# Kernel optimization log

Hardware: AMD Instinct MI355X
Metric: run time of the kernel (lower is better)

Reference implementation:

```python
import jax, jax.numpy as jnp
import numpy as np

N_WIRES = 8
DIM = 1 << N_WIRES  # 256
ENC_WIRES = [0, 1, 2, 2, 4, 5, 6, 7]  # faithful to source: wire 2 twice, wire 3 skipped

# Precompute composed CNOT-ring permutation: CNOT(0,1),(1,2),...,(6,7),(7,0)
_idx = np.arange(DIM)
_perm = _idx.copy()
for c, t in [(k, k + 1) for k in range(N_WIRES - 1)] + [(N_WIRES - 1, 0)]:
    cbit = (_idx >> (N_WIRES - 1 - c)) & 1
    P = np.where(cbit == 1, _idx ^ (1 << (N_WIRES - 1 - t)), _idx)
    _perm = _perm[P]
CNOT_PERM = jnp.asarray(_perm)
# Pauli-Z sign table per wire: (8, 256)
Z_SIGNS = jnp.asarray(1 - 2 * ((_idx[None, :] >> (N_WIRES - 1 - np.arange(N_WIRES)[:, None])) & 1)).astype(jnp.float32)


def _rx(state, wire, theta):
    """Apply RX(theta) on `wire`. state: (N, 256) complex64, theta: (N,) float."""
    N = state.shape[0]
    s = state.reshape(N, 1 << wire, 2, 1 << (N_WIRES - 1 - wire))
    half = theta * 0.5
    c = jnp.cos(half)[:, None, None]
    sn = jnp.sin(half)[:, None, None]
    a, b = s[:, :, 0, :], s[:, :, 1, :]
    top = c * a - 1j * sn * b
    bot = -1j * sn * a + c * b
    return jnp.stack([top, bot], axis=2).reshape(N, DIM)


def qlayer(tokens, theta):
    """Batched 8-qubit circuit: encoder RX(x_k), trainable RX(theta_w), CNOT ring, <Z_w>.
    tokens: (N, 8) float32 -> (N, 8) float32 expectation values."""
    N = tokens.shape[0]
    state = jnp.zeros((N, DIM), jnp.complex64).at[:, 0].set(1.0)
    for k, w in enumerate(ENC_WIRES):
        state = _rx(state, w, tokens[:, k])
    for w in range(N_WIRES):
        state = _rx(state, w, jnp.broadcast_to(theta[w], (N,)))
    state = state[:, CNOT_PERM]
    probs = state.real ** 2 + state.imag ** 2  # (N, 256)
    return probs @ Z_SIGNS.T  # (N, 8)


def setup_inputs() -> dict:
    key = jax.random.key(0)
    kx, kt = jax.random.split(key)
    x = jax.random.normal(kx, (16, 1024, 8), dtype=jnp.float32)
    theta = jax.random.uniform(kt, (8,), dtype=jnp.float32, minval=0.0, maxval=2.0 * np.pi)
    return {"x": x, "theta": theta}


def reference(x, theta):
    B, S, E = x.shape
    H, dk = 2, E // 2
    tok = x.reshape(B * S, E)
    # Original computes Q, K, V with the SAME shared q_layer on the SAME input,
    # so Q == K == V; compute once.
    qkv = qlayer(tok, theta).reshape(B, S, E)
    h = qkv.reshape(B, S, H, dk).transpose(0, 2, 1, 3)  # (B,H,S,dk)
    scores = jnp.einsum('bhqd,bhkd->bhqk', h, h) / np.sqrt(dk).astype(np.float32)
    w = jax.nn.softmax(scores, axis=-1)  # (eval mode: dropout inactive)
    attn = jnp.einsum('bhqk,bhkd->bhqd', w, h)
    concat = attn.transpose(0, 2, 1, 3).reshape(B, S, E)
    out = qlayer(concat.reshape(B * S, E), theta).reshape(B, S, E)
    return out
```

## Files before the change

kernel.cpp:

```cpp
#include <hip/hip_runtime.h>

#define SEQ 1024

typedef __attribute__((ext_vector_type(2))) float f2;

static __device__ __forceinline__ int lds_addr(int k) {
    return (k << 3) + ((k >> 4) << 2);
}

static __device__ __forceinline__ void qrow(const float th[8], const float y[8], float o[8]) {
    float a[8];
    a[0] = y[0] + th[0];
    a[1] = y[1] + th[1];
    a[2] = y[2] + y[3] + th[2];
    a[3] = th[3];
    a[4] = y[4] + th[4];
    a[5] = y[5] + th[5];
    a[6] = y[6] + th[6];
    a[7] = y[7] + th[7];
    float c[8];
#pragma unroll
    for (int w = 0; w < 8; ++w) c[w] = __cosf(a[w]);
    o[1] = c[0] * c[1];
#pragma unroll
    for (int w = 2; w < 8; ++w) o[w] = o[w - 1] * c[w];
    float s = c[7];
#pragma unroll
    for (int w = 6; w >= 1; --w) s *= c[w];
    o[0] = s;
}

__global__ __launch_bounds__(256, 4) void mhaq_fused(const float* __restrict__ x,
                                                     const float* __restrict__ theta,
                                                     float* __restrict__ out) {
    __shared__ __align__(16) float h_lds[8448];

    const int b   = blockIdx.x >> 6;
    const int qof = (blockIdx.x & 63) << 4;
    const int t   = threadIdx.x;

    float th[8];
#pragma unroll
    for (int w = 0; w < 8; ++w) th[w] = theta[w];

    const float4* xb = (const float4*)(x + (size_t)b * SEQ * 8);
    float4 v0[4], v1[4];
#pragma unroll
    for (int r = 0; r < 4; ++r) {
        const int k = t + (r << 8);
        v0[r] = xb[2 * k];
        v1[r] = xb[2 * k + 1];
    }
#pragma unroll
    for (int r = 0; r < 4; ++r) {
        const int k = t + (r << 8);
        const float y[8] = {v0[r].x, v0[r].y, v0[r].z, v0[r].w,
                            v1[r].x, v1[r].y, v1[r].z, v1[r].w};
        float o[8];
        qrow(th, y, o);
        float4* p = (float4*)&h_lds[lds_addr(k)];
        p[0] = make_float4(o[0], o[1], o[2], o[3]);
        p[1] = make_float4(o[4], o[5], o[6], o[7]);
    }
    __syncthreads();

    const int lane  = t & 63;
    const int wv    = t >> 6;
    const int qbase = qof + (wv << 2);

    const float qscale = 0.5f * 1.44269504f;
    f2 qv[4][4];
#pragma unroll
    for (int qq = 0; qq < 4; ++qq) {
        const float* qp = &h_lds[lds_addr(qbase + qq)];
        qv[qq][0] = f2{qp[0], qp[1]} * qscale;
        qv[qq][1] = f2{qp[2], qp[3]} * qscale;
        qv[qq][2] = f2{qp[4], qp[5]} * qscale;
        qv[qq][3] = f2{qp[6], qp[7]} * qscale;
    }

    float l0[4] = {0.f, 0.f, 0.f, 0.f};
    float l1[4] = {0.f, 0.f, 0.f, 0.f};
    f2 a01[4], a23[4], a45[4], a67[4];
#pragma unroll
    for (int qq = 0; qq < 4; ++qq) {
        a01[qq] = f2{0.f, 0.f};
        a23[qq] = f2{0.f, 0.f};
        a45[qq] = f2{0.f, 0.f};
        a67[qq] = f2{0.f, 0.f};
    }

    int base = lds_addr(lane << 4);
#pragma unroll 4
    for (int i = 0; i < 16; ++i) {
        const float4 k0 = *(const float4*)&h_lds[base];
        const float4 k1 = *(const float4*)&h_lds[base + 4];
        base += 8;
        const f2 k01 = {k0.x, k0.y}, k23 = {k0.z, k0.w};
        const f2 k45 = {k1.x, k1.y}, k67 = {k1.z, k1.w};
#pragma unroll
        for (int qq = 0; qq < 4; ++qq) {
            const f2 d0 = qv[qq][0] * k01 + qv[qq][1] * k23;
            const f2 d1 = qv[qq][2] * k45 + qv[qq][3] * k67;
            const float e0 = __builtin_amdgcn_exp2f(d0.x + d0.y);
            const float e1 = __builtin_amdgcn_exp2f(d1.x + d1.y);
            l0[qq] += e0;
            l1[qq] += e1;
            const f2 e0v = {e0, e0}, e1v = {e1, e1};
            a01[qq] += e0v * k01;
            a23[qq] += e0v * k23;
            a45[qq] += e1v * k45;
            a67[qq] += e1v * k67;
        }
    }

    float red[40];
#pragma unroll
    for (int qq = 0; qq < 4; ++qq) {
        red[qq * 10 + 0] = l0[qq];
        red[qq * 10 + 1] = l1[qq];
        red[qq * 10 + 2] = a01[qq].x;
        red[qq * 10 + 3] = a01[qq].y;
        red[qq * 10 + 4] = a23[qq].x;
        red[qq * 10 + 5] = a23[qq].y;
        red[qq * 10 + 6] = a45[qq].x;
        red[qq * 10 + 7] = a45[qq].y;
        red[qq * 10 + 8] = a67[qq].x;
        red[qq * 10 + 9] = a67[qq].y;
    }
#pragma unroll
    for (int m = 1; m < 64; m <<= 1) {
#pragma unroll
        for (int j = 0; j < 40; ++j) red[j] += __shfl_xor(red[j], m);
    }

    float sel[10];
#pragma unroll
    for (int j = 0; j < 10; ++j) {
        const float v01 = (lane & 1) ? red[10 + j] : red[j];
        const float v23 = (lane & 1) ? red[30 + j] : red[20 + j];
        sel[j] = (lane & 2) ? v23 : v01;
    }
    if (lane < 4) {
        const float inv0 = 1.0f / sel[0];
        const float inv1 = 1.0f / sel[1];
        float y[8];
#pragma unroll
        for (int d = 0; d < 4; ++d) {
            y[d]     = sel[2 + d] * inv0;
            y[4 + d] = sel[6 + d] * inv1;
        }
        float o[8];
        qrow(th, y, o);
        float4* op = (float4*)(out + ((size_t)(b * SEQ + qbase + lane)) * 8);
        op[0] = make_float4(o[0], o[1], o[2], o[3]);
        op[1] = make_float4(o[4], o[5], o[6], o[7]);
    }
}

extern "C" void kernel_launch(void* const* d_in, const int* in_sizes, int n_in,
                              void* d_out, int out_size, void* d_ws, size_t ws_size,
                              hipStream_t stream) {
    const float* x     = (const float*)d_in[0];
    const float* theta = (const float*)d_in[1];
    float* out         = (float*)d_out;
    mhaq_fused<<<dim3(16 * 64), dim3(256), 0, stream>>>(x, theta, out);
}
```

Before: 69.92 us.

## Double queries per block, split keys across lanes, reduce partials through LDS

Each block now handles 32 queries instead of 16, so the per-block recomputation of the first quantum layer over all 1024 keys is amortised over twice as many queries and the grid is halved. Within a wave, each group of 16 lanes owns 4 queries, and each lane covers a 32-key slice within half of the keys. The 64-lane shuffle butterfly over 40 values is replaced by a staged LDS write plus a cross-thread summation. An XOR-swizzled slot layout replaces the padded layout to avoid bank conflicts. The cost is more LDS use (about 46 KB), lower occupancy hint (2 blocks per SM), and extra barriers.

```diff
diff --git a/kernel.cpp b/kernel.cpp
--- a/kernel.cpp
+++ b/kernel.cpp
@@ -4,8 +4,8 @@
 
 typedef __attribute__((ext_vector_type(2))) float f2;
 
-static __device__ __forceinline__ int lds_addr(int k) {
-    return (k << 3) + ((k >> 4) << 2);
+static __device__ __forceinline__ int slot_addr(int s) {
+    return (s ^ ((s >> 6) & 7)) << 2;
 }
 
 static __device__ __forceinline__ void qrow(const float th[8], const float y[8], float o[8]) {
@@ -30,13 +30,14 @@
     o[0] = s;
 }
 
-__global__ __launch_bounds__(256, 4) void mhaq_fused(const float* __restrict__ x,
+__global__ __launch_bounds__(256, 2) void mhaq_fused(const float* __restrict__ x,
                                                      const float* __restrict__ theta,
                                                      float* __restrict__ out) {
-    __shared__ __align__(16) float h_lds[8448];
+    __shared__ __align__(16) float smem[11264 + 320];
+    float* const res = smem + 11264;
 
-    const int b   = blockIdx.x >> 6;
-    const int qof = (blockIdx.x & 63) << 4;
+    const int b   = blockIdx.x >> 5;
+    const int qof = (blockIdx.x & 31) << 5;
     const int t   = threadIdx.x;
 
     float th[8];
@@ -58,25 +59,29 @@
                             v1[r].x, v1[r].y, v1[r].z, v1[r].w};
         float o[8];
         qrow(th, y, o);
-        float4* p = (float4*)&h_lds[lds_addr(k)];
-        p[0] = make_float4(o[0], o[1], o[2], o[3]);
-        p[1] = make_float4(o[4], o[5], o[6], o[7]);
+        *(float4*)&smem[slot_addr(2 * k)]     = make_float4(o[0], o[1], o[2], o[3]);
+        *(float4*)&smem[slot_addr(2 * k + 1)] = make_float4(o[4], o[5], o[6], o[7]);
     }
     __syncthreads();
 
-    const int lane  = t & 63;
-    const int wv    = t >> 6;
-    const int qbase = qof + (wv << 2);
+    const int lane = t & 63;
+    const int wv   = t >> 6;
+    const int qs   = wv >> 1;
+    const int kh   = wv & 1;
+    const int g    = lane >> 4;
+    const int m    = lane & 15;
+    const int q0   = qof + (qs << 4) + (g << 2);
 
     const float qscale = 0.5f * 1.44269504f;
     f2 qv[4][4];
 #pragma unroll
     for (int qq = 0; qq < 4; ++qq) {
-        const float* qp = &h_lds[lds_addr(qbase + qq)];
-        qv[qq][0] = f2{qp[0], qp[1]} * qscale;
-        qv[qq][1] = f2{qp[2], qp[3]} * qscale;
-        qv[qq][2] = f2{qp[4], qp[5]} * qscale;
-        qv[qq][3] = f2{qp[6], qp[7]} * qscale;
+        const float4 qa = *(const float4*)&smem[slot_addr(2 * (q0 + qq))];
+        const float4 qb = *(const float4*)&smem[slot_addr(2 * (q0 + qq) + 1)];
+        qv[qq][0] = f2{qa.x, qa.y} * qscale;
+        qv[qq][1] = f2{qa.z, qa.w} * qscale;
+        qv[qq][2] = f2{qb.x, qb.y} * qscale;
+        qv[qq][3] = f2{qb.z, qb.w} * qscale;
     }
 
     float l0[4] = {0.f, 0.f, 0.f, 0.f};
@@ -90,12 +95,12 @@
         a67[qq] = f2{0.f, 0.f};
     }
 
-    int base = lds_addr(lane << 4);
+    const int kbase = (kh << 9) + (m << 5);
 #pragma unroll 4
-    for (int i = 0; i < 16; ++i) {
-        const float4 k0 = *(const float4*)&h_lds[base];
-        const float4 k1 = *(const float4*)&h_lds[base + 4];
-        base += 8;
+    for (int i = 0; i < 32; ++i) {
+        const int s0 = (kbase + i) << 1;
+        const float4 k0 = *(const float4*)&smem[slot_addr(s0)];
+        const float4 k1 = *(const float4*)&smem[slot_addr(s0 + 1)];
         const f2 k01 = {k0.x, k0.y}, k23 = {k0.z, k0.w};
         const f2 k45 = {k1.x, k1.y}, k67 = {k1.z, k1.w};
 #pragma unroll
@@ -113,46 +118,51 @@
             a67[qq] += e1v * k67;
         }
     }
+    __syncthreads();
 
-    float red[40];
+    {
+        float buf[40];
 #pragma unroll
-    for (int qq = 0; qq < 4; ++qq) {
-        red[qq * 10 + 0] = l0[qq];
-        red[qq * 10 + 1] = l1[qq];
-        red[qq * 10 + 2] = a01[qq].x;
-        red[qq * 10 + 3] = a01[qq].y;
-        red[qq * 10 + 4] = a23[qq].x;
-        red[qq * 10 + 5] = a23[qq].y;
-        red[qq * 10 + 6] = a45[qq].x;
-        red[qq * 10 + 7] = a45[qq].y;
-        red[qq * 10 + 8] = a67[qq].x;
-        red[qq * 10 + 9] = a67[qq].y;
+        for (int qq = 0; qq < 4; ++qq) {
+            buf[qq * 10 + 0] = l0[qq];
+            buf[qq * 10 + 1] = l1[qq];
+            buf[qq * 10 + 2] = a01[qq].x;
+            buf[qq * 10 + 3] = a01[qq].y;
+            buf[qq * 10 + 4] = a23[qq].x;
+            buf[qq * 10 + 5] = a23[qq].y;
+            buf[qq * 10 + 6] = a45[qq].x;
+            buf[qq * 10 + 7] = a45[qq].y;
+            buf[qq * 10 + 8] = a67[qq].x;
+            buf[qq * 10 + 9] = a67[qq].y;
+        }
+        float4* pp = (float4*)&smem[t * 44];
+#pragma unroll
+        for (int i = 0; i < 10; ++i) pp[i] = ((const float4*)buf)[i];
     }
+    __syncthreads();
+
+    for (int u = t; u < 320; u += 256) {
+        const int q  = u / 10;
+        const int j  = u - q * 10;
+        const int uqs = q >> 4, ug = (q >> 2) & 3, uqq = q & 3;
+        const int base = ((uqs << 7) + (ug << 4)) * 44 + uqq * 10 + j;
+        float s = 0.f;
 #pragma unroll
-    for (int m = 1; m < 64; m <<= 1) {
-#pragma unroll
-        for (int j = 0; j < 40; ++j) red[j] += __shfl_xor(red[j], m);
+        for (int mm = 0; mm < 16; ++mm)
+            s += smem[base + mm * 44] + smem[base + (64 + mm) * 44];
+        res[q * 10 + j] = s;
     }
+    __syncthreads();
 
-    float sel[10];
-#pragma unroll
-    for (int j = 0; j < 10; ++j) {
-        const float v01 = (lane & 1) ? red[10 + j] : red[j];
-        const float v23 = (lane & 1) ? red[30 + j] : red[20 + j];
-        sel[j] = (lane & 2) ? v23 : v01;
-    }
-    if (lane < 4) {
-        const float inv0 = 1.0f / sel[0];
-        const float inv1 = 1.0f / sel[1];
-        float y[8];
-#pragma unroll
-        for (int d = 0; d < 4; ++d) {
-            y[d]     = sel[2 + d] * inv0;
-            y[4 + d] = sel[6 + d] * inv1;
-        }
+    if (t < 32) {
+        const float* r = &res[t * 10];
+        const float inv0 = 1.0f / r[0];
+        const float inv1 = 1.0f / r[1];
+        const float y[8] = {r[2] * inv0, r[3] * inv0, r[4] * inv0, r[5] * inv0,
+                            r[6] * inv1, r[7] * inv1, r[8] * inv1, r[9] * inv1};
         float o[8];
         qrow(th, y, o);
-        float4* op = (float4*)(out + ((size_t)(b * SEQ + qbase + lane)) * 8);
+        float4* op = (float4*)(out + ((size_t)(b * SEQ + qof + t)) * 8);
         op[0] = make_float4(o[0], o[1], o[2], o[3]);
         op[1] = make_float4(o[4], o[5], o[6], o[7]);
     }
@@ -164,5 +174,5 @@
     const float* x     = (const float*)d_in[0];
     const float* theta = (const float*)d_in[1];
     float* out         = (float*)d_out;
-    mhaq_fused<<<dim3(16 * 64), dim3(256), 0, stream>>>(x, theta, out);
+    mhaq_fused<<<dim3(512), dim3(256), 0, stream>>>(x, theta, out);
 }
```

Result: faster. 66.47 us (-4.9%).
